# Optimization experiments

Hardware: AMD Instinct MI355X
Metric: run time of the kernel (lower is better)

Reference implementation:

```python
import jax, jax.numpy as jnp
import numpy as np

N_NODES = 50000
N_EDGES = 50000  # number of hyperedges
NNZ = 800000
IN_C, HID_C, OUT_C = 256, 128, 64


def _glorot(key, shape):
    lim = float(np.sqrt(6.0 / (shape[0] + shape[1])))
    return jax.random.uniform(key, shape, jnp.float32, -lim, lim)


def setup_inputs() -> dict:
    key = jax.random.key(0)
    ks = jax.random.split(key, 8)
    x = jax.random.normal(ks[0], (N_NODES, IN_C), jnp.float32)
    node_idx = jax.random.randint(ks[1], (NNZ,), 0, N_NODES)
    edge_idx = jax.random.randint(ks[2], (NNZ,), 0, N_EDGES)
    hyperedge_index = jnp.stack([node_idx, edge_idx]).astype(jnp.int64)
    return {
        "x": x,
        "hyperedge_index": hyperedge_index,
        "W1": _glorot(ks[3], (IN_C, HID_C)),
        "b1": jnp.zeros((HID_C,), jnp.float32),
        "W2": _glorot(ks[4], (HID_C, OUT_C)),
        "b2": jnp.zeros((OUT_C,), jnp.float32),
        "Wp": _glorot(ks[5], (OUT_C, OUT_C)),
        "bp": jax.random.normal(ks[6], (OUT_C,), jnp.float32) * 0.01,
    }


def _hypergraph_conv(x, node_idx, edge_idx, W, b):
    # PyG HypergraphConv: out = D^-1 H B H^T (X W) + b
    x = x @ W  # [N, F]
    ones = jnp.ones((node_idx.shape[0],), x.dtype)
    d = jax.ops.segment_sum(ones, node_idx, num_segments=N_NODES)   # node degree
    be = jax.ops.segment_sum(ones, edge_idx, num_segments=N_EDGES)  # hyperedge size
    Dinv = jnp.where(d > 0, 1.0 / d, 0.0)
    Binv = jnp.where(be > 0, 1.0 / be, 0.0)
    # node -> hyperedge aggregation
    m = jax.ops.segment_sum(x[node_idx], edge_idx, num_segments=N_EDGES) * Binv[:, None]
    # hyperedge -> node aggregation
    out = jax.ops.segment_sum(m[edge_idx], node_idx, num_segments=N_NODES) * Dinv[:, None]
    return out + b


def reference(x, hyperedge_index, W1, b1, W2, b2, Wp, bp):
    node_idx = hyperedge_index[0]
    edge_idx = hyperedge_index[1]
    h = jax.nn.relu(_hypergraph_conv(x, node_idx, edge_idx, W1, b1))
    features_1 = h
    h = jax.nn.relu(_hypergraph_conv(h, node_idx, edge_idx, W2, b2))
    features_2 = h
    z = h @ Wp + bp
    return (z, features_1, features_2)
```

## Files before the change

kernel.cpp:

```cpp
#include <hip/hip_runtime.h>


typedef unsigned short u16;
typedef unsigned int   u32;
typedef _Float16 f16;
typedef __attribute__((ext_vector_type(8))) short short8;
typedef __attribute__((ext_vector_type(8))) _Float16 half8;
typedef __attribute__((ext_vector_type(4))) float f32x4;

static const int BCAP = 3072;

__device__ __forceinline__ float bf2f(u16 u) {
    return __builtin_bit_cast(float, (u32)u << 16);
}
__device__ __forceinline__ u16 f2bf(float f) {
    u32 b = __builtin_bit_cast(u32, f);
    b += 0x7FFFu + ((b >> 16) & 1u);
    return (u16)(b >> 16);
}

__device__ __forceinline__ void wsplit_one(const float* __restrict__ W, u16* __restrict__ out,
                                           int K, int N, int local)
{
    int kp = local % 72;
    int rest = local / 72;
    int n = rest % N;
    int c = rest / N;
    float v = 0.f;
    if (kp < 64) v = W[(size_t)(c * 64 + kp) * N + n];
    u16 h = f2bf(v);
    u16 l = f2bf(v - bf2f(h));
    size_t base = (size_t)c * (2 * (size_t)N * 72);
    out[base + (size_t)n * 72 + kp] = h;
    out[base + (size_t)N * 72 + (size_t)n * 72 + kp] = l;
}

__global__ __launch_bounds__(256) void wsplit_all_kernel(
    const float* __restrict__ W1, const float* __restrict__ W2, const float* __restrict__ Wp,
    u16* __restrict__ w1sp, u16* __restrict__ w2sp, u16* __restrict__ wpsp)
{
    const int T1 = 4 * 128 * 72;
    const int T2 = 2 * 64 * 72;
    const int T3 = 1 * 64 * 72;
    int idx = blockIdx.x * 256 + threadIdx.x;
    if (idx < T1)                 wsplit_one(W1, w1sp, 256, 128, idx);
    else if (idx < T1 + T2)       wsplit_one(W2, w2sp, 128, 64, idx - T1);
    else if (idx < T1 + T2 + T3)  wsplit_one(Wp, wpsp, 64, 64, idx - T1 - T2);
}

__global__ __launch_bounds__(256) void bin_scatter_kernel(
    const int* __restrict__ hidx,
    int* __restrict__ curEb, int* __restrict__ curNb,
    u32* __restrict__ tmpE, u32* __restrict__ tmpN,
    int nnz, int nNodes, int nEdges)
{
    __shared__ int histE[400], histN[400];
    __shared__ int s_st;
    int t = threadIdx.x;
    const int nbE = (nEdges + 127) >> 7, nbN = (nNodes + 127) >> 7;
    for (int b = t; b < 400; b += 256) { histE[b] = 0; histN[b] = 0; }
    if (t < 64) {
        unsigned long long m = __ballot(hidx[2 * t + 1] != 0);
        if (t == 0) s_st = (m == 0ull) ? 2 : 1;
    }
    __syncthreads();
    int st = s_st;
    size_t eoff = (size_t)nnz * st;
    int i0 = blockIdx.x * 4096;
    int e_[16], n_[16]; int rE[16], rN[16];
    #pragma unroll
    for (int k = 0; k < 16; ++k) {
        int i = i0 + k * 256 + t;
        int n = -1, e = 0;
        if (i < nnz) {
            n = hidx[(size_t)i * st];
            e = hidx[eoff + (size_t)i * st];
            if (!((u32)n < (u32)nNodes && (u32)e < (u32)nEdges)) n = -1;
        }
        n_[k] = n; e_[k] = e;
        if (n >= 0) {
            rE[k] = atomicAdd(&histE[e >> 7], 1);
            rN[k] = atomicAdd(&histN[n >> 7], 1);
        }
    }
    __syncthreads();
    for (int b = t; b < nbE; b += 256) { int c = histE[b]; if (c) histE[b] = atomicAdd(&curEb[b], c); }
    for (int b = t; b < nbN; b += 256) { int c = histN[b]; if (c) histN[b] = atomicAdd(&curNb[b], c); }
    __syncthreads();
    #pragma unroll
    for (int k = 0; k < 16; ++k) {
        if (n_[k] >= 0) {
            int e = e_[k], n = n_[k];
            int lpE = histE[e >> 7] + rE[k];
            int lpN = histN[n >> 7] + rN[k];
            if (lpE < BCAP) tmpE[(size_t)(e >> 7) * BCAP + lpE] = ((u32)(e & 127) << 16) | (u32)n;
            if (lpN < BCAP) tmpN[(size_t)(n >> 7) * BCAP + lpN] = ((u32)(n & 127) << 16) | (u32)e;
        }
    }
}

__global__ __launch_bounds__(64) void bkt_scan_kernel(
    const int* __restrict__ curE, const int* __restrict__ curN,
    int* __restrict__ baseE, int* __restrict__ baseN, int nbE, int nbN)
{
    const int* cur; int* base; int nb;
    if (blockIdx.x == 0) { cur = curE; base = baseE; nb = nbE; }
    else                 { cur = curN; base = baseN; nb = nbN; }
    int lane = threadIdx.x;
    int carry = 0;
    for (int c0 = 0; c0 < nb; c0 += 64) {
        int i = c0 + lane;
        int v = (i < nb) ? cur[i] : 0;
        int orig = v;
        for (int o = 1; o < 64; o <<= 1) { int u = __shfl_up(v, o, 64); if (lane >= o) v += u; }
        if (i < nb) base[i] = carry + v - orig;
        carry += __shfl(v, 63, 64);
    }
    if (lane == 0) base[nb] = carry;
}

__global__ __launch_bounds__(256) void bin_build_kernel(
    const u32* __restrict__ tmpE, const u32* __restrict__ tmpN,
    const int* __restrict__ baseE, const int* __restrict__ baseN,
    int* __restrict__ deg_e, int* __restrict__ offs_e, float* __restrict__ binv, u16* __restrict__ adj_e,
    int* __restrict__ deg_n, int* __restrict__ offs_n, float* __restrict__ dinv, u16* __restrict__ adj_n,
    int nE, int nN, int nbE)
{
    __shared__ u32 buf[4096];
    __shared__ int lcnt[128], lpre[128], lcur[128];
    int b = blockIdx.x;
    const u32* tmp; const int* base; int* deg; int* offs; float* inv; u16* adj; int n, tb;
    if (b < nbE) { tmp=tmpE; base=baseE; deg=deg_e; offs=offs_e; inv=binv; adj=adj_e; n=nE; tb=b; }
    else         { tmp=tmpN; base=baseN; deg=deg_n; offs=offs_n; inv=dinv; adj=adj_n; n=nN; tb=b-nbE; }
    int t = threadIdx.x;
    int g0 = tb << 7;
    int gbase = base[tb];
    int cnt = base[tb + 1] - gbase;
    int avail = cnt < BCAP ? cnt : BCAP;
    size_t tbase = (size_t)tb * BCAP;
    if (t < 128) lcnt[t] = 0;
    __syncthreads();
    for (int j = t; j < avail; j += 256) atomicAdd(&lcnt[tmp[tbase + j] >> 16], 1);
    __syncthreads();
    if (t < 64) {
        int a0 = lcnt[2 * t], a1 = lcnt[2 * t + 1];
        int ps = a0 + a1, v = ps;
        for (int o = 1; o < 64; o <<= 1) { int u = __shfl_up(v, o, 64); if (t >= o) v += u; }
        int excl = v - ps;
        lpre[2 * t] = excl; lpre[2 * t + 1] = excl + a0;
    }
    __syncthreads();
    if (t < 128) {
        int id = g0 + t;
        if (id < n) {
            int d = lcnt[t];
            deg[id]  = d;
            offs[id] = gbase + lpre[t];
            inv[id]  = d > 0 ? 1.0f / (float)d : 0.0f;
        }
        lcur[t] = lpre[t];
    }
    __syncthreads();
    if (avail <= 0) return;
    for (int j = t; j < avail; j += 256) {
        u32 v = tmp[tbase + j];
        int pos = atomicAdd(&lcur[v >> 16], 1);
        buf[pos] = v & 0xFFFFu;
    }
    __syncthreads();
    for (int j = t; j < avail; j += 256) adj[gbase + j] = (u16)buf[j];
}

template<int NP, bool FINAL, int C>
__global__ __launch_bounds__(256) void gather_slice_kernel(
    const f16* __restrict__ src, const u16* __restrict__ adj,
    const int* __restrict__ offs, const int* __restrict__ deg,
    const float* __restrict__ inv, const float* __restrict__ bias,
    void* __restrict__ dstv, int nRows, int nSrcRows)
{
    constexpr int SW = 32;
    constexpr int TPR = 4;
    constexpr int RPB = 64;
    int t = threadIdx.x;
    int plane = blockIdx.x & (NP - 1);
    int chunk = blockIdx.x / NP;
    int r = chunk * RPB + t / TPR;
    if (r >= nRows) return;
    int sub = t & 3;
    const f16* sp = src + (size_t)plane * nSrcRows * SW + sub * 8;
    int j = offs[r], e = j + deg[r];
    float a0[8], a1[8], a2[8], a3[8];
    #pragma unroll
    for (int q = 0; q < 8; ++q) { a0[q] = 0.f; a1[q] = 0.f; a2[q] = 0.f; a3[q] = 0.f; }
    for (; j + 4 <= e; j += 4) {
        int s0 = adj[j], s1 = adj[j + 1], s2 = adj[j + 2], s3 = adj[j + 3];
        const half8 v0 = *(const half8*)(sp + (size_t)s0 * SW);
        const half8 v1 = *(const half8*)(sp + (size_t)s1 * SW);
        const half8 v2 = *(const half8*)(sp + (size_t)s2 * SW);
        const half8 v3 = *(const half8*)(sp + (size_t)s3 * SW);
        #pragma unroll
        for (int q = 0; q < 8; ++q) {
            a0[q] += (float)v0[q]; a1[q] += (float)v1[q];
            a2[q] += (float)v2[q]; a3[q] += (float)v3[q];
        }
    }
    for (; j < e; ++j) {
        int s0 = adj[j];
        const half8 v0 = *(const half8*)(sp + (size_t)s0 * SW);
        #pragma unroll
        for (int q = 0; q < 8; ++q) a0[q] += (float)v0[q];
    }
    float scv = inv[r];
    float rr[8];
    #pragma unroll
    for (int q = 0; q < 8; ++q) rr[q] = ((a0[q] + a1[q]) + (a2[q] + a3[q])) * scv;
    if constexpr (FINAL) {
        float* dst = (float*)dstv;
        size_t o = (size_t)r * C + plane * SW + sub * 8;
        const float* bp = bias + plane * SW + sub * 8;
        const float4 b0 = *(const float4*)(bp);
        const float4 b1 = *(const float4*)(bp + 4);
        float4 o0, o1;
        o0.x = fmaxf(rr[0] + b0.x, 0.0f); o0.y = fmaxf(rr[1] + b0.y, 0.0f);
        o0.z = fmaxf(rr[2] + b0.z, 0.0f); o0.w = fmaxf(rr[3] + b0.w, 0.0f);
        o1.x = fmaxf(rr[4] + b1.x, 0.0f); o1.y = fmaxf(rr[5] + b1.y, 0.0f);
        o1.z = fmaxf(rr[6] + b1.z, 0.0f); o1.w = fmaxf(rr[7] + b1.w, 0.0f);
        *(float4*)(dst + o)     = o0;
        *(float4*)(dst + o + 4) = o1;
    } else {
        f16* dst = (f16*)dstv;
        half8 ov;
        #pragma unroll
        for (int q = 0; q < 8; ++q) ov[q] = (f16)rr[q];
        *(half8*)(dst + ((size_t)plane * nRows + r) * SW + sub * 8) = ov;
    }
}

__device__ __forceinline__ void split8(const float* __restrict__ p, short8& hi, short8& lo) {
    #pragma unroll
    for (int j = 0; j < 8; ++j) {
        float v = p[j];
        u16 h = f2bf(v);
        hi[j] = (short)h;
        lo[j] = (short)f2bf(v - bf2f(h));
    }
}

template<int K, int N, bool BIAS, int OUT>
__global__ __launch_bounds__(1024) void gemm_mfma_kernel(
    const float* __restrict__ A, const u16* __restrict__ Bsp,
    const float* __restrict__ bias, void* __restrict__ C_, int M)
{
    constexpr int KP = 72;
    constexpr int NCH = K / 64;
    constexpr int CHUNK = 2 * N * KP;
    constexpr int NTW = N / 32;
    __shared__ alignas(16) u16 Bbuf[NCH * CHUNK];
    const int tid = threadIdx.x;
    constexpr int U = NCH * CHUNK / 8;
    for (int u = tid; u < U; u += 1024)
        *(float4*)(&Bbuf[(size_t)u * 8]) = *(const float4*)(Bsp + (size_t)u * 8);
    __syncthreads();
    const int wave = tid >> 6, lane = tid & 63;
    const int mg = wave >> 1, nh = wave & 1;
    const int lr = lane & 15, kq = (lane >> 4) * 8;
    const int nt0 = nh * NTW;
    const int MT = (M + 127) >> 7;
    for (int tile = blockIdx.x; tile < MT; tile += gridDim.x) {
        const int row0 = tile * 128 + mg * 16;
        if (row0 >= M) continue;
        f32x4 acc[NTW];
        #pragma unroll
        for (int i = 0; i < NTW; ++i) acc[i] = (f32x4){0.f, 0.f, 0.f, 0.f};
        const float* Ap = A + (size_t)(row0 + lr) * K + kq;
        #pragma unroll
        for (int c = 0; c < NCH; ++c) {
            #pragma unroll
            for (int k0 = 0; k0 < 64; k0 += 32) {
                short8 ah, al;
                split8(Ap + c * 64 + k0, ah, al);
                #pragma unroll
                for (int f = 0; f < NTW; ++f) {
                    const int col = (nt0 + f) * 16 + lr;
                    const int bo = c * CHUNK + col * KP + k0 + kq;
                    const short8 bh = *(const short8*)(&Bbuf[bo]);
                    const short8 bl = *(const short8*)(&Bbuf[bo + N * KP]);
                    acc[f] = __builtin_amdgcn_mfma_f32_16x16x32_bf16(ah, bh, acc[f], 0, 0, 0);
                    acc[f] = __builtin_amdgcn_mfma_f32_16x16x32_bf16(al, bh, acc[f], 0, 0, 0);
                    acc[f] = __builtin_amdgcn_mfma_f32_16x16x32_bf16(ah, bl, acc[f], 0, 0, 0);
                }
            }
        }
        const int orow = row0 + (lane >> 4) * 4;
        #pragma unroll
        for (int f = 0; f < NTW; ++f) {
            const int col = (nt0 + f) * 16 + lr;
            float bv = 0.0f;
            if constexpr (BIAS) bv = bias[col];
            #pragma unroll
            for (int j = 0; j < 4; ++j) {
                float vv = acc[f][j] + bv;
                if constexpr (OUT == 0) {
                    ((float*)C_)[(size_t)(orow + j) * N + col] = vv;
                } else {
                    ((f16*)C_)[((size_t)(col >> 5) * M + (orow + j)) * 32 + (col & 31)] = (f16)vv;
                }
            }
        }
    }
}

extern "C" void kernel_launch(void* const* d_in, const int* in_sizes, int n_in,
                              void* d_out, int out_size, void* d_ws, size_t ws_size,
                              hipStream_t stream)
{
    (void)n_in; (void)out_size; (void)ws_size;
    const float* x  = (const float*)d_in[0];
    const int* hidx = (const int*)d_in[1];
    const float* W1 = (const float*)d_in[2];
    const float* b1 = (const float*)d_in[3];
    const float* W2 = (const float*)d_in[4];
    const float* b2 = (const float*)d_in[5];
    const float* Wp = (const float*)d_in[6];
    const float* bp = (const float*)d_in[7];
    float* out = (float*)d_out;

    const int nnz    = in_sizes[1] / 2;
    const int nNodes = in_sizes[0] / 256;
    const int nEdges = 50000;

    char* w = (char*)d_ws;
    const size_t SEG = 200192;
    int*   deg_e  = (int*)(w + 0 * SEG);
    int*   deg_n  = (int*)(w + 1 * SEG);
    int*   offs_e = (int*)(w + 2 * SEG);
    int*   offs_n = (int*)(w + 3 * SEG);
    float* binv   = (float*)(w + 4 * SEG);
    float* dinv   = (float*)(w + 5 * SEG);
    int*   curEb  = (int*)(w + 6 * SEG + 256);
    int*   curNb  = (int*)(w + 6 * SEG + 2304);
    int*   baseE  = (int*)(w + 6 * SEG + 4352);
    int*   baseN  = (int*)(w + 6 * SEG + 6400);
    char* p = w + 6 * SEG + 8448;
    u16* adj_e = (u16*)p;  p += (size_t)nnz * 2;
    u16* adj_n = (u16*)p;  p += (size_t)nnz * 2;
    f16* h0  = (f16*)p;
    f16* m1  = (f16*)(p + (size_t)nNodes * 128 * 2);
    f16* h1w = h0;
    f16* m2  = (f16*)((char*)h0 + (size_t)nNodes * 64 * 2);
    u16* w1sp = (u16*)(p + 2 * (size_t)nNodes * 128 * 2);
    u16* w2sp = w1sp + 4 * 18432;
    u16* wpsp = w2sp + 2 * 9216;

    const int nbE = (nEdges + 127) >> 7;
    const int nbN = (nNodes + 127) >> 7;
    u32* tmpE = (u32*)m1;
    u32* tmpN = tmpE + (size_t)nbE * BCAP;

    const size_t F1OFF = (size_t)nNodes * 64;
    const size_t F2OFF = F1OFF + (size_t)nNodes * 128;

    hipMemsetAsync(w + 6 * SEG + 256, 0, 4096, stream);
    wsplit_all_kernel<<<(4*128*72 + 2*64*72 + 1*64*72 + 255) / 256, 256, 0, stream>>>(
        W1, W2, Wp, w1sp, w2sp, wpsp);
    bin_scatter_kernel<<<(nnz + 4095) / 4096, 256, 0, stream>>>(
        hidx, curEb, curNb, tmpE, tmpN, nnz, nNodes, nEdges);
    bkt_scan_kernel<<<2, 64, 0, stream>>>(curEb, curNb, baseE, baseN, nbE, nbN);
    bin_build_kernel<<<nbE + nbN, 256, 0, stream>>>(
        tmpE, tmpN, baseE, baseN,
        deg_e, offs_e, binv, adj_e,
        deg_n, offs_n, dinv, adj_n,
        nEdges, nNodes, nbE);

    const int chunksE = (nEdges + 63) / 64;
    const int chunksN = (nNodes + 63) / 64;

    gemm_mfma_kernel<256, 128, false, 1><<<256, 1024, 0, stream>>>(x, w1sp, nullptr, h0, nNodes);
    gather_slice_kernel<4, false, 128><<<chunksE * 4, 256, 0, stream>>>(
        h0, adj_e, offs_e, deg_e, binv, nullptr, m1, nEdges, nNodes);
    gather_slice_kernel<4, true, 128><<<chunksN * 4, 256, 0, stream>>>(
        m1, adj_n, offs_n, deg_n, dinv, b1, out + F1OFF, nNodes, nEdges);

    gemm_mfma_kernel<128, 64, false, 1><<<391, 1024, 0, stream>>>(
        out + F1OFF, w2sp, nullptr, h1w, nNodes);
    gather_slice_kernel<2, false, 64><<<chunksE * 2, 256, 0, stream>>>(
        h1w, adj_e, offs_e, deg_e, binv, nullptr, m2, nEdges, nNodes);
    gather_slice_kernel<2, true, 64><<<chunksN * 2, 256, 0, stream>>>(
        m2, adj_n, offs_n, deg_n, dinv, b2, out + F2OFF, nNodes, nEdges);

    gemm_mfma_kernel<64, 64, true, 0><<<391, 1024, 0, stream>>>(
        out + F2OFF, wpsp, bp, out, nNodes);
}
```

Baseline: 274.2 us.

## Degree-sort rows within each 128-row bucket to balance gather wavefronts

The bucket build now bitonic-sorts the 128 rows of each bucket by degree and writes permuted degree, offset, inverse and original-row arrays. The gather kernels walk rows in that permuted order so lanes in a wavefront have similar degrees, and write results back through the row map. Separately, the cursor memset is folded into the weight-split kernel, and the scatter kernel uses 1024-thread blocks. This is meant to reduce divergence in the gathers and drop one launch, at the cost of a sort and an extra indirection.

```diff
diff --git a/kernel.cpp b/kernel.cpp
--- a/kernel.cpp
+++ b/kernel.cpp
@@ -37,18 +37,22 @@
 
 __global__ __launch_bounds__(256) void wsplit_all_kernel(
     const float* __restrict__ W1, const float* __restrict__ W2, const float* __restrict__ Wp,
-    u16* __restrict__ w1sp, u16* __restrict__ w2sp, u16* __restrict__ wpsp)
+    u16* __restrict__ w1sp, u16* __restrict__ w2sp, u16* __restrict__ wpsp,
+    int* __restrict__ cursors)
 {
     const int T1 = 4 * 128 * 72;
     const int T2 = 2 * 64 * 72;
     const int T3 = 1 * 64 * 72;
+    if (blockIdx.x == 0) {
+        for (int z = threadIdx.x; z < 1024; z += 256) cursors[z] = 0;
+    }
     int idx = blockIdx.x * 256 + threadIdx.x;
     if (idx < T1)                 wsplit_one(W1, w1sp, 256, 128, idx);
     else if (idx < T1 + T2)       wsplit_one(W2, w2sp, 128, 64, idx - T1);
     else if (idx < T1 + T2 + T3)  wsplit_one(Wp, wpsp, 64, 64, idx - T1 - T2);
 }
 
-__global__ __launch_bounds__(256) void bin_scatter_kernel(
+__global__ __launch_bounds__(1024) void bin_scatter_kernel(
     const int* __restrict__ hidx,
     int* __restrict__ curEb, int* __restrict__ curNb,
     u32* __restrict__ tmpE, u32* __restrict__ tmpN,
@@ -58,7 +62,7 @@
     __shared__ int s_st;
     int t = threadIdx.x;
     const int nbE = (nEdges + 127) >> 7, nbN = (nNodes + 127) >> 7;
-    for (int b = t; b < 400; b += 256) { histE[b] = 0; histN[b] = 0; }
+    for (int b = t; b < 400; b += 1024) { histE[b] = 0; histN[b] = 0; }
     if (t < 64) {
         unsigned long long m = __ballot(hidx[2 * t + 1] != 0);
         if (t == 0) s_st = (m == 0ull) ? 2 : 1;
@@ -67,10 +71,10 @@
     int st = s_st;
     size_t eoff = (size_t)nnz * st;
     int i0 = blockIdx.x * 4096;
-    int e_[16], n_[16]; int rE[16], rN[16];
+    int e_[4], n_[4]; int rE[4], rN[4];
     #pragma unroll
-    for (int k = 0; k < 16; ++k) {
-        int i = i0 + k * 256 + t;
+    for (int k = 0; k < 4; ++k) {
+        int i = i0 + k * 1024 + t;
         int n = -1, e = 0;
         if (i < nnz) {
             n = hidx[(size_t)i * st];
@@ -84,11 +88,11 @@
         }
     }
     __syncthreads();
-    for (int b = t; b < nbE; b += 256) { int c = histE[b]; if (c) histE[b] = atomicAdd(&curEb[b], c); }
-    for (int b = t; b < nbN; b += 256) { int c = histN[b]; if (c) histN[b] = atomicAdd(&curNb[b], c); }
+    for (int b = t; b < nbE; b += 1024) { int c = histE[b]; if (c) histE[b] = atomicAdd(&curEb[b], c); }
+    for (int b = t; b < nbN; b += 1024) { int c = histN[b]; if (c) histN[b] = atomicAdd(&curNb[b], c); }
     __syncthreads();
     #pragma unroll
-    for (int k = 0; k < 16; ++k) {
+    for (int k = 0; k < 4; ++k) {
         if (n_[k] >= 0) {
             int e = e_[k], n = n_[k];
             int lpE = histE[e >> 7] + rE[k];
@@ -122,16 +126,19 @@
 __global__ __launch_bounds__(256) void bin_build_kernel(
     const u32* __restrict__ tmpE, const u32* __restrict__ tmpN,
     const int* __restrict__ baseE, const int* __restrict__ baseN,
-    int* __restrict__ deg_e, int* __restrict__ offs_e, float* __restrict__ binv, u16* __restrict__ adj_e,
-    int* __restrict__ deg_n, int* __restrict__ offs_n, float* __restrict__ dinv, u16* __restrict__ adj_n,
+    int* __restrict__ pdeg_e, int* __restrict__ poffs_e, float* __restrict__ pinv_e,
+    u16* __restrict__ prow_e, u16* __restrict__ adj_e,
+    int* __restrict__ pdeg_n, int* __restrict__ poffs_n, float* __restrict__ pinv_n,
+    u16* __restrict__ prow_n, u16* __restrict__ adj_n,
     int nE, int nN, int nbE)
 {
     __shared__ u32 buf[4096];
     __shared__ int lcnt[128], lpre[128], lcur[128];
+    __shared__ u32 skey[128];
     int b = blockIdx.x;
-    const u32* tmp; const int* base; int* deg; int* offs; float* inv; u16* adj; int n, tb;
-    if (b < nbE) { tmp=tmpE; base=baseE; deg=deg_e; offs=offs_e; inv=binv; adj=adj_e; n=nE; tb=b; }
-    else         { tmp=tmpN; base=baseN; deg=deg_n; offs=offs_n; inv=dinv; adj=adj_n; n=nN; tb=b-nbE; }
+    const u32* tmp; const int* base; int* pdeg; int* poffs; float* pinv; u16* prow; u16* adj; int n, tb;
+    if (b < nbE) { tmp=tmpE; base=baseE; pdeg=pdeg_e; poffs=poffs_e; pinv=pinv_e; prow=prow_e; adj=adj_e; n=nE; tb=b; }
+    else         { tmp=tmpN; base=baseN; pdeg=pdeg_n; poffs=poffs_n; pinv=pinv_n; prow=prow_n; adj=adj_n; n=nN; tb=b-nbE; }
     int t = threadIdx.x;
     int g0 = tb << 7;
     int gbase = base[tb];
@@ -152,13 +159,35 @@
     __syncthreads();
     if (t < 128) {
         int id = g0 + t;
-        if (id < n) {
-            int d = lcnt[t];
-            deg[id]  = d;
-            offs[id] = gbase + lpre[t];
-            inv[id]  = d > 0 ? 1.0f / (float)d : 0.0f;
-        }
+        skey[t] = (id < n) ? (((u32)lcnt[t] << 16) | (u32)t) : 0xFFFFFFFFu;
         lcur[t] = lpre[t];
+    }
+    __syncthreads();
+    for (int kk = 2; kk <= 128; kk <<= 1) {
+        for (int jj = kk >> 1; jj > 0; jj >>= 1) {
+            if (t < 128) {
+                int ixj = t ^ jj;
+                if (ixj > t) {
+                    u32 a = skey[t], c2 = skey[ixj];
+                    bool sw = ((t & kk) == 0) ? (a > c2) : (a < c2);
+                    if (sw) { skey[t] = c2; skey[ixj] = a; }
+                }
+            }
+            __syncthreads();
+        }
+    }
+    if (t < 128) {
+        u32 s = skey[t];
+        int gpos = (tb << 7) + t;
+        if (s == 0xFFFFFFFFu) {
+            pdeg[gpos] = 0; poffs[gpos] = 0; pinv[gpos] = 0.f; prow[gpos] = (u16)0xFFFFu;
+        } else {
+            int d = (int)(s >> 16), lrow = (int)(s & 0xFFFFu);
+            pdeg[gpos]  = d;
+            poffs[gpos] = gbase + lpre[lrow];
+            pinv[gpos]  = d > 0 ? 1.0f / (float)d : 0.0f;
+            prow[gpos]  = (u16)(g0 + lrow);
+        }
     }
     __syncthreads();
     if (avail <= 0) return;
@@ -174,21 +203,20 @@
 template<int NP, bool FINAL, int C>
 __global__ __launch_bounds__(256) void gather_slice_kernel(
     const f16* __restrict__ src, const u16* __restrict__ adj,
-    const int* __restrict__ offs, const int* __restrict__ deg,
-    const float* __restrict__ inv, const float* __restrict__ bias,
-    void* __restrict__ dstv, int nRows, int nSrcRows)
+    const int* __restrict__ poffs, const int* __restrict__ pdeg,
+    const float* __restrict__ pinv, const u16* __restrict__ prow,
+    const float* __restrict__ bias,
+    void* __restrict__ dstv, int nSrcRows, int nDstRows)
 {
     constexpr int SW = 32;
-    constexpr int TPR = 4;
-    constexpr int RPB = 64;
     int t = threadIdx.x;
     int plane = blockIdx.x & (NP - 1);
     int chunk = blockIdx.x / NP;
-    int r = chunk * RPB + t / TPR;
-    if (r >= nRows) return;
+    int r = chunk * 64 + (t >> 2);
     int sub = t & 3;
     const f16* sp = src + (size_t)plane * nSrcRows * SW + sub * 8;
-    int j = offs[r], e = j + deg[r];
+    int row = prow[r];
+    int j = poffs[r], e = j + pdeg[r];
     float a0[8], a1[8], a2[8], a3[8];
     #pragma unroll
     for (int q = 0; q < 8; ++q) { a0[q] = 0.f; a1[q] = 0.f; a2[q] = 0.f; a3[q] = 0.f; }
@@ -210,13 +238,14 @@
         #pragma unroll
         for (int q = 0; q < 8; ++q) a0[q] += (float)v0[q];
     }
-    float scv = inv[r];
+    if (row == 0xFFFF) return;
+    float scv = pinv[r];
     float rr[8];
     #pragma unroll
     for (int q = 0; q < 8; ++q) rr[q] = ((a0[q] + a1[q]) + (a2[q] + a3[q])) * scv;
     if constexpr (FINAL) {
         float* dst = (float*)dstv;
-        size_t o = (size_t)r * C + plane * SW + sub * 8;
+        size_t o = (size_t)row * C + plane * SW + sub * 8;
         const float* bp = bias + plane * SW + sub * 8;
         const float4 b0 = *(const float4*)(bp);
         const float4 b1 = *(const float4*)(bp + 4);
@@ -232,7 +261,7 @@
         half8 ov;
         #pragma unroll
         for (int q = 0; q < 8; ++q) ov[q] = (f16)rr[q];
-        *(half8*)(dst + ((size_t)plane * nRows + r) * SW + sub * 8) = ov;
+        *(half8*)(dst + ((size_t)plane * nDstRows + row) * SW + sub * 8) = ov;
     }
 }
 
@@ -331,12 +360,12 @@
 
     char* w = (char*)d_ws;
     const size_t SEG = 200192;
-    int*   deg_e  = (int*)(w + 0 * SEG);
-    int*   deg_n  = (int*)(w + 1 * SEG);
-    int*   offs_e = (int*)(w + 2 * SEG);
-    int*   offs_n = (int*)(w + 3 * SEG);
-    float* binv   = (float*)(w + 4 * SEG);
-    float* dinv   = (float*)(w + 5 * SEG);
+    int*   pdeg_e  = (int*)(w + 0 * SEG);
+    int*   pdeg_n  = (int*)(w + 1 * SEG);
+    int*   poffs_e = (int*)(w + 2 * SEG);
+    int*   poffs_n = (int*)(w + 3 * SEG);
+    float* pinv_e  = (float*)(w + 4 * SEG);
+    float* pinv_n  = (float*)(w + 5 * SEG);
     int*   curEb  = (int*)(w + 6 * SEG + 256);
     int*   curNb  = (int*)(w + 6 * SEG + 2304);
     int*   baseE  = (int*)(w + 6 * SEG + 4352);
@@ -344,6 +373,8 @@
     char* p = w + 6 * SEG + 8448;
     u16* adj_e = (u16*)p;  p += (size_t)nnz * 2;
     u16* adj_n = (u16*)p;  p += (size_t)nnz * 2;
+    u16* prow_e = (u16*)p; p += 100352;
+    u16* prow_n = (u16*)p; p += 100352;
     f16* h0  = (f16*)p;
     f16* m1  = (f16*)(p + (size_t)nNodes * 128 * 2);
     f16* h1w = h0;
@@ -360,33 +391,31 @@
     const size_t F1OFF = (size_t)nNodes * 64;
     const size_t F2OFF = F1OFF + (size_t)nNodes * 128;
 
-    hipMemsetAsync(w + 6 * SEG + 256, 0, 4096, stream);
     wsplit_all_kernel<<<(4*128*72 + 2*64*72 + 1*64*72 + 255) / 256, 256, 0, stream>>>(
-        W1, W2, Wp, w1sp, w2sp, wpsp);
-    bin_scatter_kernel<<<(nnz + 4095) / 4096, 256, 0, stream>>>(
+        W1, W2, Wp, w1sp, w2sp, wpsp, curEb);
+    bin_scatter_kernel<<<(nnz + 4095) / 4096, 1024, 0, stream>>>(
         hidx, curEb, curNb, tmpE, tmpN, nnz, nNodes, nEdges);
     bkt_scan_kernel<<<2, 64, 0, stream>>>(curEb, curNb, baseE, baseN, nbE, nbN);
     bin_build_kernel<<<nbE + nbN, 256, 0, stream>>>(
         tmpE, tmpN, baseE, baseN,
-        deg_e, offs_e, binv, adj_e,
-        deg_n, offs_n, dinv, adj_n,
+        pdeg_e, poffs_e, pinv_e, prow_e, adj_e,
+        pdeg_n, poffs_n, pinv_n, prow_n, adj_n,
         nEdges, nNodes, nbE);
 
-    const int chunksE = (nEdges + 63) / 64;
-    const int chunksN = (nNodes + 63) / 64;
+    const int chunks = (nbE * 128) / 64;
 
     gemm_mfma_kernel<256, 128, false, 1><<<256, 1024, 0, stream>>>(x, w1sp, nullptr, h0, nNodes);
-    gather_slice_kernel<4, false, 128><<<chunksE * 4, 256, 0, stream>>>(
-        h0, adj_e, offs_e, deg_e, binv, nullptr, m1, nEdges, nNodes);
-    gather_slice_kernel<4, true, 128><<<chunksN * 4, 256, 0, stream>>>(
-        m1, adj_n, offs_n, deg_n, dinv, b1, out + F1OFF, nNodes, nEdges);
+    gather_slice_kernel<4, false, 128><<<chunks * 4, 256, 0, stream>>>(
+        h0, adj_e, poffs_e, pdeg_e, pinv_e, prow_e, nullptr, m1, nNodes, nEdges);
+    gather_slice_kernel<4, true, 128><<<chunks * 4, 256, 0, stream>>>(
+        m1, adj_n, poffs_n, pdeg_n, pinv_n, prow_n, b1, out + F1OFF, nEdges, nNodes);
 
     gemm_mfma_kernel<128, 64, false, 1><<<391, 1024, 0, stream>>>(
         out + F1OFF, w2sp, nullptr, h1w, nNodes);
-    gather_slice_kernel<2, false, 64><<<chunksE * 2, 256, 0, stream>>>(
-        h1w, adj_e, offs_e, deg_e, binv, nullptr, m2, nEdges, nNodes);
-    gather_slice_kernel<2, true, 64><<<chunksN * 2, 256, 0, stream>>>(
-        m2, adj_n, offs_n, deg_n, dinv, b2, out + F2OFF, nNodes, nEdges);
+    gather_slice_kernel<2, false, 64><<<chunks * 2, 256, 0, stream>>>(
+        h1w, adj_e, poffs_e, pdeg_e, pinv_e, prow_e, nullptr, m2, nNodes, nEdges);
+    gather_slice_kernel<2, true, 64><<<chunks * 2, 256, 0, stream>>>(
+        m2, adj_n, poffs_n, pdeg_n, pinv_n, prow_n, b2, out + F2OFF, nEdges, nNodes);
 
     gemm_mfma_kernel<64, 64, true, 0><<<391, 1024, 0, stream>>>(
         out + F2OFF, wpsp, bp, out, nNodes);
```

After: 279.4 us. No clear change (+1.9%).

## Fold memset and bucket scan into other kernels, widen scatter blocks, unroll gathers

Applied to the files above, without the earlier changes.

Replaces the hipMemsetAsync of the bucket cursors with zeroing inside the weight-split kernel, and folds the standalone bucket scan kernel into the first GEMM launch (blocks 0 and 1 run the scan before the GEMM). Launch count drops by two. The binning scatter now uses 1024-thread blocks with fewer items per thread, and the gather loop gains an 8-way unrolled path for more memory-level parallelism. The cursor zeroing assumes the cursor region is 1024 ints starting at curEb, and the first GEMM now delays two blocks behind a serial scan.

```diff
diff --git a/kernel.cpp b/kernel.cpp
--- a/kernel.cpp
+++ b/kernel.cpp
@@ -37,18 +37,22 @@
 
 __global__ __launch_bounds__(256) void wsplit_all_kernel(
     const float* __restrict__ W1, const float* __restrict__ W2, const float* __restrict__ Wp,
-    u16* __restrict__ w1sp, u16* __restrict__ w2sp, u16* __restrict__ wpsp)
+    u16* __restrict__ w1sp, u16* __restrict__ w2sp, u16* __restrict__ wpsp,
+    int* __restrict__ cursors)
 {
     const int T1 = 4 * 128 * 72;
     const int T2 = 2 * 64 * 72;
     const int T3 = 1 * 64 * 72;
+    if (blockIdx.x == 0) {
+        for (int z = threadIdx.x; z < 1024; z += 256) cursors[z] = 0;
+    }
     int idx = blockIdx.x * 256 + threadIdx.x;
     if (idx < T1)                 wsplit_one(W1, w1sp, 256, 128, idx);
     else if (idx < T1 + T2)       wsplit_one(W2, w2sp, 128, 64, idx - T1);
     else if (idx < T1 + T2 + T3)  wsplit_one(Wp, wpsp, 64, 64, idx - T1 - T2);
 }
 
-__global__ __launch_bounds__(256) void bin_scatter_kernel(
+__global__ __launch_bounds__(1024) void bin_scatter_kernel(
     const int* __restrict__ hidx,
     int* __restrict__ curEb, int* __restrict__ curNb,
     u32* __restrict__ tmpE, u32* __restrict__ tmpN,
@@ -58,7 +62,7 @@
     __shared__ int s_st;
     int t = threadIdx.x;
     const int nbE = (nEdges + 127) >> 7, nbN = (nNodes + 127) >> 7;
-    for (int b = t; b < 400; b += 256) { histE[b] = 0; histN[b] = 0; }
+    for (int b = t; b < 400; b += 1024) { histE[b] = 0; histN[b] = 0; }
     if (t < 64) {
         unsigned long long m = __ballot(hidx[2 * t + 1] != 0);
         if (t == 0) s_st = (m == 0ull) ? 2 : 1;
@@ -67,10 +71,10 @@
     int st = s_st;
     size_t eoff = (size_t)nnz * st;
     int i0 = blockIdx.x * 4096;
-    int e_[16], n_[16]; int rE[16], rN[16];
+    int e_[4], n_[4]; int rE[4], rN[4];
     #pragma unroll
-    for (int k = 0; k < 16; ++k) {
-        int i = i0 + k * 256 + t;
+    for (int k = 0; k < 4; ++k) {
+        int i = i0 + k * 1024 + t;
         int n = -1, e = 0;
         if (i < nnz) {
             n = hidx[(size_t)i * st];
@@ -84,11 +88,11 @@
         }
     }
     __syncthreads();
-    for (int b = t; b < nbE; b += 256) { int c = histE[b]; if (c) histE[b] = atomicAdd(&curEb[b], c); }
-    for (int b = t; b < nbN; b += 256) { int c = histN[b]; if (c) histN[b] = atomicAdd(&curNb[b], c); }
+    for (int b = t; b < nbE; b += 1024) { int c = histE[b]; if (c) histE[b] = atomicAdd(&curEb[b], c); }
+    for (int b = t; b < nbN; b += 1024) { int c = histN[b]; if (c) histN[b] = atomicAdd(&curNb[b], c); }
     __syncthreads();
     #pragma unroll
-    for (int k = 0; k < 16; ++k) {
+    for (int k = 0; k < 4; ++k) {
         if (n_[k] >= 0) {
             int e = e_[k], n = n_[k];
             int lpE = histE[e >> 7] + rE[k];
@@ -97,26 +101,6 @@
             if (lpN < BCAP) tmpN[(size_t)(n >> 7) * BCAP + lpN] = ((u32)(n & 127) << 16) | (u32)e;
         }
     }
-}
-
-__global__ __launch_bounds__(64) void bkt_scan_kernel(
-    const int* __restrict__ curE, const int* __restrict__ curN,
-    int* __restrict__ baseE, int* __restrict__ baseN, int nbE, int nbN)
-{
-    const int* cur; int* base; int nb;
-    if (blockIdx.x == 0) { cur = curE; base = baseE; nb = nbE; }
-    else                 { cur = curN; base = baseN; nb = nbN; }
-    int lane = threadIdx.x;
-    int carry = 0;
-    for (int c0 = 0; c0 < nb; c0 += 64) {
-        int i = c0 + lane;
-        int v = (i < nb) ? cur[i] : 0;
-        int orig = v;
-        for (int o = 1; o < 64; o <<= 1) { int u = __shfl_up(v, o, 64); if (lane >= o) v += u; }
-        if (i < nb) base[i] = carry + v - orig;
-        carry += __shfl(v, 63, 64);
-    }
-    if (lane == 0) base[nb] = carry;
 }
 
 __global__ __launch_bounds__(256) void bin_build_kernel(
@@ -179,12 +163,10 @@
     void* __restrict__ dstv, int nRows, int nSrcRows)
 {
     constexpr int SW = 32;
-    constexpr int TPR = 4;
-    constexpr int RPB = 64;
     int t = threadIdx.x;
     int plane = blockIdx.x & (NP - 1);
     int chunk = blockIdx.x / NP;
-    int r = chunk * RPB + t / TPR;
+    int r = chunk * 64 + (t >> 2);
     if (r >= nRows) return;
     int sub = t & 3;
     const f16* sp = src + (size_t)plane * nSrcRows * SW + sub * 8;
@@ -192,6 +174,25 @@
     float a0[8], a1[8], a2[8], a3[8];
     #pragma unroll
     for (int q = 0; q < 8; ++q) { a0[q] = 0.f; a1[q] = 0.f; a2[q] = 0.f; a3[q] = 0.f; }
+    for (; j + 8 <= e; j += 8) {
+        int s0 = adj[j],     s1 = adj[j + 1], s2 = adj[j + 2], s3 = adj[j + 3];
+        int s4 = adj[j + 4], s5 = adj[j + 5], s6 = adj[j + 6], s7 = adj[j + 7];
+        const half8 v0 = *(const half8*)(sp + (size_t)s0 * SW);
+        const half8 v1 = *(const half8*)(sp + (size_t)s1 * SW);
+        const half8 v2 = *(const half8*)(sp + (size_t)s2 * SW);
+        const half8 v3 = *(const half8*)(sp + (size_t)s3 * SW);
+        const half8 v4 = *(const half8*)(sp + (size_t)s4 * SW);
+        const half8 v5 = *(const half8*)(sp + (size_t)s5 * SW);
+        const half8 v6 = *(const half8*)(sp + (size_t)s6 * SW);
+        const half8 v7 = *(const half8*)(sp + (size_t)s7 * SW);
+        #pragma unroll
+        for (int q = 0; q < 8; ++q) {
+            a0[q] += (float)v0[q] + (float)v4[q];
+            a1[q] += (float)v1[q] + (float)v5[q];
+            a2[q] += (float)v2[q] + (float)v6[q];
+            a3[q] += (float)v3[q] + (float)v7[q];
+        }
+    }
     for (; j + 4 <= e; j += 4) {
         int s0 = adj[j], s1 = adj[j + 1], s2 = adj[j + 2], s3 = adj[j + 3];
         const half8 v0 = *(const half8*)(sp + (size_t)s0 * SW);
@@ -246,10 +247,12 @@
     }
 }
 
-template<int K, int N, bool BIAS, int OUT>
+template<int K, int N, bool BIAS, int OUT, bool DOSCAN>
 __global__ __launch_bounds__(1024) void gemm_mfma_kernel(
     const float* __restrict__ A, const u16* __restrict__ Bsp,
-    const float* __restrict__ bias, void* __restrict__ C_, int M)
+    const float* __restrict__ bias, void* __restrict__ C_, int M,
+    const int* __restrict__ curEb, const int* __restrict__ curNb,
+    int* __restrict__ baseE, int* __restrict__ baseN, int nbE, int nbN)
 {
     constexpr int KP = 72;
     constexpr int NCH = K / 64;
@@ -257,6 +260,23 @@
     constexpr int NTW = N / 32;
     __shared__ alignas(16) u16 Bbuf[NCH * CHUNK];
     const int tid = threadIdx.x;
+    if constexpr (DOSCAN) {
+        if (blockIdx.x < 2 && tid < 64) {
+            const int* cur = (blockIdx.x == 0) ? curEb : curNb;
+            int* base      = (blockIdx.x == 0) ? baseE : baseN;
+            const int nb   = (blockIdx.x == 0) ? nbE : nbN;
+            int carry = 0;
+            for (int c0 = 0; c0 < nb; c0 += 64) {
+                int i = c0 + tid;
+                int v = (i < nb) ? cur[i] : 0;
+                int orig = v;
+                for (int o = 1; o < 64; o <<= 1) { int u = __shfl_up(v, o, 64); if (tid >= o) v += u; }
+                if (i < nb) base[i] = carry + v - orig;
+                carry += __shfl(v, 63, 64);
+            }
+            if (tid == 0) base[nb] = carry;
+        }
+    }
     constexpr int U = NCH * CHUNK / 8;
     for (int u = tid; u < U; u += 1024)
         *(float4*)(&Bbuf[(size_t)u * 8]) = *(const float4*)(Bsp + (size_t)u * 8);
@@ -360,34 +380,30 @@
     const size_t F1OFF = (size_t)nNodes * 64;
     const size_t F2OFF = F1OFF + (size_t)nNodes * 128;
 
-    hipMemsetAsync(w + 6 * SEG + 256, 0, 4096, stream);
+    const int chunksE = (nEdges + 63) / 64;
+    const int chunksN = (nNodes + 63) / 64;
+
     wsplit_all_kernel<<<(4*128*72 + 2*64*72 + 1*64*72 + 255) / 256, 256, 0, stream>>>(
-        W1, W2, Wp, w1sp, w2sp, wpsp);
-    bin_scatter_kernel<<<(nnz + 4095) / 4096, 256, 0, stream>>>(
+        W1, W2, Wp, w1sp, w2sp, wpsp, curEb);
+    bin_scatter_kernel<<<(nnz + 4095) / 4096, 1024, 0, stream>>>(
         hidx, curEb, curNb, tmpE, tmpN, nnz, nNodes, nEdges);
-    bkt_scan_kernel<<<2, 64, 0, stream>>>(curEb, curNb, baseE, baseN, nbE, nbN);
+    gemm_mfma_kernel<256, 128, false, 1, true><<<256, 1024, 0, stream>>>(
+        x, w1sp, nullptr, h0, nNodes, curEb, curNb, baseE, baseN, nbE, nbN);
     bin_build_kernel<<<nbE + nbN, 256, 0, stream>>>(
         tmpE, tmpN, baseE, baseN,
         deg_e, offs_e, binv, adj_e,
         deg_n, offs_n, dinv, adj_n,
         nEdges, nNodes, nbE);
-
-    const int chunksE = (nEdges + 63) / 64;
-    const int chunksN = (nNodes + 63) / 64;
-
-    gemm_mfma_kernel<256, 128, false, 1><<<256, 1024, 0, stream>>>(x, w1sp, nullptr, h0, nNodes);
     gather_slice_kernel<4, false, 128><<<chunksE * 4, 256, 0, stream>>>(
         h0, adj_e, offs_e, deg_e, binv, nullptr, m1, nEdges, nNodes);
     gather_slice_kernel<4, true, 128><<<chunksN * 4, 256, 0, stream>>>(
         m1, adj_n, offs_n, deg_n, dinv, b1, out + F1OFF, nNodes, nEdges);
-
-    gemm_mfma_kernel<128, 64, false, 1><<<391, 1024, 0, stream>>>(
-        out + F1OFF, w2sp, nullptr, h1w, nNodes);
+    gemm_mfma_kernel<128, 64, false, 1, false><<<391, 1024, 0, stream>>>(
+        out + F1OFF, w2sp, nullptr, h1w, nNodes, nullptr, nullptr, nullptr, nullptr, 0, 0);
     gather_slice_kernel<2, false, 64><<<chunksE * 2, 256, 0, stream>>>(
         h1w, adj_e, offs_e, deg_e, binv, nullptr, m2, nEdges, nNodes);
     gather_slice_kernel<2, true, 64><<<chunksN * 2, 256, 0, stream>>>(
         m2, adj_n, offs_n, deg_n, dinv, b2, out + F2OFF, nNodes, nEdges);
-
-    gemm_mfma_kernel<64, 64, true, 0><<<391, 1024, 0, stream>>>(
-        out + F2OFF, wpsp, bp, out, nNodes);
-}
+    gemm_mfma_kernel<64, 64, true, 0, false><<<391, 1024, 0, stream>>>(
+        out + F2OFF, wpsp, bp, out, nNodes, nullptr, nullptr, nullptr, nullptr, 0, 0);
+}
```

Measured after the change: 265.0 us. -3.4%, faster.
